# Performance work log

Measured on AMD Instinct MI355X. Metric: run time of the kernel, lower is better.

## Reference

```python
import jax, jax.numpy as jnp
import numpy as np


def setup_inputs() -> dict:
    key = jax.random.key(0)
    k1, k2 = jax.random.split(key)
    B, S, D, R = 8, 2048, 1024, 128
    batch = jax.random.normal(k1, (B, S, D), dtype=jnp.float32)
    proj = jax.random.normal(k2, (D, R), dtype=jnp.float32) * (1.0 / np.sqrt(D))
    return {"batch": batch, "proj": proj}


def reference(batch, proj):
    # transformed: (B, S, R)
    t = jnp.matmul(batch, proj)
    # Pairwise squared L2 distances: ||ti||^2 + ||tj||^2 - 2 ti.tj
    # (same math as expand/diff/pow/sum, without the (B,S,S,R) intermediate)
    sq = jnp.sum(t * t, axis=-1)                       # (B, S)
    dots = jnp.einsum('bir,bjr->bij', t, t)            # (B, S, S)
    d2 = sq[:, :, None] + sq[:, None, :] - 2.0 * dots  # (B, S, S)
    return d2
```

## Files before the change

kernel.cpp:

```cpp
#include <hip/hip_runtime.h>
#include <hip/hip_bf16.h>

typedef short bf16x8 __attribute__((ext_vector_type(8)));
typedef float f32x4 __attribute__((ext_vector_type(4)));

#define NB 8
#define SS 2048
#define DD 1024
#define RR 128

__device__ __forceinline__ short f2bf(float x){
  unsigned u = __float_as_uint(x);
  u += 0x7fffu + ((u >> 16) & 1u);
  return (short)(u >> 16);
}
__device__ __forceinline__ float bf2f(short h){
  return __uint_as_float(((unsigned)(unsigned short)h) << 16);
}
__device__ __forceinline__ void gload16(const void* g, void* l){
  __builtin_amdgcn_global_load_lds((const __attribute__((address_space(1))) unsigned*)g,
                                   (__attribute__((address_space(3))) unsigned*)l, 16, 0, 0);
}
__device__ __forceinline__ int swz(int row, int c16){
  return row * 64 + ((c16 ^ (row & 7)) << 3);
}

__global__ __launch_bounds__(256) void k0_proj(const float* __restrict__ proj,
                                               short* __restrict__ pt_hi,
                                               short* __restrict__ pt_lo){
  __shared__ float tile[64][65];
  const int d0 = blockIdx.x * 64, r0 = blockIdx.y * 64;
  const int tid = threadIdx.x;
  #pragma unroll
  for (int i = 0; i < 16; ++i){
    int u = i * 256 + tid;
    int d = u >> 6, r = u & 63;
    tile[d][r] = proj[(d0 + d) * RR + r0 + r];
  }
  __syncthreads();
  #pragma unroll
  for (int i = 0; i < 16; ++i){
    int u = i * 256 + tid;
    int r = u >> 6, d = u & 63;
    float x = tile[d][r];
    short h = f2bf(x);
    short l = f2bf(x - bf2f(h));
    pt_hi[(r0 + r) * DD + d0 + d] = h;
    pt_lo[(r0 + r) * DD + d0 + d] = l;
  }
}

__global__ __launch_bounds__(512, 2) void k1_gemm1(const float* __restrict__ batch,
                                                   const short* __restrict__ pt_hi,
                                                   const short* __restrict__ pt_lo,
                                                   short* __restrict__ t_hi,
                                                   float* __restrict__ sqv){
  __shared__ __align__(16) char smem[49408];
  short* Ah = (short*)smem;
  short* Al = (short*)(smem + 8192);
  short* Ph = (short*)(smem + 16384);
  short* Pl = (short*)(smem + 32768);
  float* sqpart = (float*)(smem + 49152);
  const int tid = threadIdx.x;
  const int w = tid >> 6, lane = tid & 63;
  const int lr = lane & 15, lg = lane >> 4;
  const int wr = w & 3, wc = w >> 2;
  const int row0 = blockIdx.x * 64;
  const int colg = (lane & 7) ^ (lane >> 3);
  if (tid < 64) sqpart[tid] = 0.f;
  f32x4 acc[4] = {{0.f,0.f,0.f,0.f}};
  #pragma unroll 1
  for (int k0 = 0; k0 < DD; k0 += 64){
    #pragma unroll
    for (int i = 0; i < 2; ++i){
      int u = tid * 2 + i;
      int r = u >> 4, kc = (u & 15) * 4;
      float4 v = *(const float4*)(batch + (size_t)(row0 + r) * DD + k0 + kc);
      short4 hv, lv;
      hv.x = f2bf(v.x); lv.x = f2bf(v.x - bf2f(hv.x));
      hv.y = f2bf(v.y); lv.y = f2bf(v.y - bf2f(hv.y));
      hv.z = f2bf(v.z); lv.z = f2bf(v.z - bf2f(hv.z));
      hv.w = f2bf(v.w); lv.w = f2bf(v.w - bf2f(hv.w));
      int sidx = r * 64 + (((kc >> 3) ^ (r & 7)) << 3) + (kc & 7);
      *(short4*)&Ah[sidx] = hv;
      *(short4*)&Al[sidx] = lv;
    }
    #pragma unroll
    for (int q = 0; q < 2; ++q){
      int prow = w * 16 + q * 8 + (lane >> 3);
      gload16(pt_hi + prow * DD + k0 + colg * 8, &Ph[w * 1024 + q * 512]);
      gload16(pt_lo + prow * DD + k0 + colg * 8, &Pl[w * 1024 + q * 512]);
    }
    __syncthreads();
    #pragma unroll
    for (int ks = 0; ks < 2; ++ks){
      int c16 = ks * 4 + lg;
      bf16x8 ah = *(const bf16x8*)&Ah[swz(wr * 16 + lr, c16)];
      bf16x8 al = *(const bf16x8*)&Al[swz(wr * 16 + lr, c16)];
      bf16x8 bh[4], bl[4];
      #pragma unroll
      for (int n = 0; n < 4; ++n){
        int prow = wc * 64 + n * 16 + lr;
        bh[n] = *(const bf16x8*)&Ph[swz(prow, c16)];
        bl[n] = *(const bf16x8*)&Pl[swz(prow, c16)];
      }
      #pragma unroll
      for (int n = 0; n < 4; ++n)
        acc[n] = __builtin_amdgcn_mfma_f32_16x16x32_bf16(ah, bh[n], acc[n], 0, 0, 0);
      #pragma unroll
      for (int n = 0; n < 4; ++n)
        acc[n] = __builtin_amdgcn_mfma_f32_16x16x32_bf16(ah, bl[n], acc[n], 0, 0, 0);
      #pragma unroll
      for (int n = 0; n < 4; ++n)
        acc[n] = __builtin_amdgcn_mfma_f32_16x16x32_bf16(al, bh[n], acc[n], 0, 0, 0);
    }
    __syncthreads();
  }
  short* Th = Ph;
  #pragma unroll
  for (int r = 0; r < 4; ++r){
    int lrow = wr * 16 + lg * 4 + r;
    float s = 0.f;
    #pragma unroll
    for (int n = 0; n < 4; ++n){
      float x = acc[n][r];
      s += x * x;
      int col = wc * 64 + n * 16 + lr;
      Th[lrow * 128 + col] = f2bf(x);
    }
    s += __shfl_xor(s, 1);
    s += __shfl_xor(s, 2);
    s += __shfl_xor(s, 4);
    s += __shfl_xor(s, 8);
    if (lr == 0) atomicAdd(&sqpart[lrow], s);
  }
  __syncthreads();
  #pragma unroll
  for (int ps = 0; ps < 2; ++ps){
    int u = ps * 512 + tid;
    int row = u >> 4, c8 = (u & 15) * 8;
    *(int4*)&t_hi[(size_t)(row0 + row) * RR + c8] = *(int4*)&Th[row * 128 + c8];
  }
  if (tid < 64) sqv[row0 + tid] = sqpart[tid];
}

__global__ __launch_bounds__(512, 4) void k2_dist(const short* __restrict__ t_hi,
                                                  const float* __restrict__ sqv,
                                                  float* __restrict__ out){
  __shared__ __align__(16) short lds[32768];
  float* ftile = (float*)lds;
  const int tid = threadIdx.x;
  const int w = tid >> 6, lane = tid & 63;
  const int lr = lane & 15, lg = lane >> 4;
  const int bi = blockIdx.x;
  int p = blockIdx.y;
  int ti = 0;
  while (p >= 16 - ti){ p -= 16 - ti; ++ti; }
  const int tj = ti + p;
  const int i0 = ti * 128, j0 = tj * 128;
  const bool dg = (ti == tj);
  const size_t tbase = (size_t)bi * SS * RR;
  float* outb = out + (size_t)bi * SS * SS;
  const float* sqb = sqv + bi * SS;
  const int srow = ((w & 1) << 2) | (lane >> 4);
  const int colg = (lane & 15) ^ srow;

  #pragma unroll
  for (int q = 0; q < 4; ++q){
    int rl = q * 32 + w * 4;
    int gr = rl + (lane >> 4);
    gload16(t_hi + tbase + (size_t)(i0 + gr) * RR + colg * 8, &lds[rl * 128]);
    if (!dg)
      gload16(t_hi + tbase + (size_t)(j0 + gr) * RR + colg * 8, &lds[16384 + rl * 128]);
  }
  __syncthreads();

  const int bh0 = dg ? 0 : 16384;
  f32x4 acc[8] = {{0.f,0.f,0.f,0.f}};
  const int ar = w * 16 + lr;
  const int aoff = ar * 128;
  const int asw = ar & 7;
  #pragma unroll
  for (int ks = 0; ks < 4; ++ks){
    int c16 = ks * 4 + lg;
    bf16x8 ah = *(const bf16x8*)&lds[aoff + ((c16 ^ asw) << 3)];
    bf16x8 bh[8];
    #pragma unroll
    for (int n = 0; n < 8; ++n){
      int br = n * 16 + lr;
      bh[n] = *(const bf16x8*)&lds[bh0 + br * 128 + ((c16 ^ (br & 7)) << 3)];
    }
    #pragma unroll
    for (int n = 0; n < 8; ++n)
      acc[n] = __builtin_amdgcn_mfma_f32_16x16x32_bf16(ah, bh[n], acc[n], 0, 0, 0);
  }
  __syncthreads();

  if (!dg){
    int rbase = w * 16 + lg * 4;
    float4 si4 = *(const float4*)&sqb[i0 + rbase];
    #pragma unroll
    for (int n = 0; n < 8; ++n){
      int col = n * 16 + lr;
      float sj = sqb[j0 + col];
      float4 mv;
      mv.x = si4.x + sj - 2.0f * acc[n][0];
      mv.y = si4.y + sj - 2.0f * acc[n][1];
      mv.z = si4.z + sj - 2.0f * acc[n][2];
      mv.w = si4.w + sj - 2.0f * acc[n][3];
      *(float4*)&outb[(size_t)(j0 + col) * SS + (i0 + rbase)] = mv;
    }
  }
  #pragma unroll
  for (int n = 0; n < 8; ++n)
    #pragma unroll
    for (int r = 0; r < 4; ++r)
      ftile[(w * 16 + lg * 4 + r) * 128 + n * 16 + lr] = acc[n][r];
  __syncthreads();
  #pragma unroll
  for (int v = 0; v < 8; ++v){
    int u = v * 512 + tid;
    int row = u >> 5, c4 = (u & 31) * 4;
    float4 d = *(float4*)&ftile[row * 128 + c4];
    float si = sqb[i0 + row];
    float4 sj = *(const float4*)&sqb[j0 + c4];
    float4 o;
    o.x = si + sj.x - 2.0f * d.x;
    o.y = si + sj.y - 2.0f * d.y;
    o.z = si + sj.z - 2.0f * d.z;
    o.w = si + sj.w - 2.0f * d.w;
    *(float4*)&outb[(size_t)(i0 + row) * SS + j0 + c4] = o;
  }
}

extern "C" void kernel_launch(void* const* d_in, const int* in_sizes, int n_in,
                              void* d_out, int out_size, void* d_ws, size_t ws_size,
                              hipStream_t stream) {
  const float* batch = (const float*)d_in[0];
  const float* proj  = (const float*)d_in[1];
  float* out = (float*)d_out;
  char* ws = (char*)d_ws;

  short* pt_hi = (short*)(ws);
  short* pt_lo = (short*)(ws + 262144);
  short* t_hi  = (short*)(ws + 524288);
  float* sqv   = (float*)(ws + 4718592);

  k0_proj<<<dim3(16, 2), 256, 0, stream>>>(proj, pt_hi, pt_lo);
  k1_gemm1<<<dim3(256), 512, 0, stream>>>(batch, pt_hi, pt_lo, t_hi, sqv);
  k2_dist<<<dim3(8, 136), 512, 0, stream>>>(t_hi, sqv, out);
}
```

Baseline: 207.9 us.

## Fuse three kernels into one cooperative persistent kernel with double-buffered GEMM

After: 360.7 us. 1.74x slower.

```diff
diff --git a/kernel.cpp b/kernel.cpp
--- a/kernel.cpp
+++ b/kernel.cpp
@@ -1,10 +1,12 @@
 #include <hip/hip_runtime.h>
 #include <hip/hip_bf16.h>
+#include <hip/hip_cooperative_groups.h>
+
+namespace cg = cooperative_groups;
 
 typedef short bf16x8 __attribute__((ext_vector_type(8)));
 typedef float f32x4 __attribute__((ext_vector_type(4)));
 
-#define NB 8
 #define SS 2048
 #define DD 1024
 #define RR 128
@@ -25,211 +27,238 @@
   return row * 64 + ((c16 ^ (row & 7)) << 3);
 }
 
-__global__ __launch_bounds__(256) void k0_proj(const float* __restrict__ proj,
-                                               short* __restrict__ pt_hi,
-                                               short* __restrict__ pt_lo){
-  __shared__ float tile[64][65];
-  const int d0 = blockIdx.x * 64, r0 = blockIdx.y * 64;
-  const int tid = threadIdx.x;
-  #pragma unroll
-  for (int i = 0; i < 16; ++i){
-    int u = i * 256 + tid;
-    int d = u >> 6, r = u & 63;
-    tile[d][r] = proj[(d0 + d) * RR + r0 + r];
-  }
-  __syncthreads();
-  #pragma unroll
-  for (int i = 0; i < 16; ++i){
-    int u = i * 256 + tid;
-    int r = u >> 6, d = u & 63;
-    float x = tile[d][r];
-    short h = f2bf(x);
-    short l = f2bf(x - bf2f(h));
-    pt_hi[(r0 + r) * DD + d0 + d] = h;
-    pt_lo[(r0 + r) * DD + d0 + d] = l;
-  }
-}
-
-__global__ __launch_bounds__(512, 2) void k1_gemm1(const float* __restrict__ batch,
-                                                   const short* __restrict__ pt_hi,
-                                                   const short* __restrict__ pt_lo,
-                                                   short* __restrict__ t_hi,
-                                                   float* __restrict__ sqv){
-  __shared__ __align__(16) char smem[49408];
-  short* Ah = (short*)smem;
-  short* Al = (short*)(smem + 8192);
-  short* Ph = (short*)(smem + 16384);
-  short* Pl = (short*)(smem + 32768);
-  float* sqpart = (float*)(smem + 49152);
+__global__ __launch_bounds__(512, 1) void fused_psd(
+    const float* __restrict__ batch, const float* __restrict__ proj,
+    short* __restrict__ pt_hi, short* __restrict__ pt_lo,
+    short* __restrict__ t_hi, float* __restrict__ sqv,
+    float* __restrict__ out){
+  __shared__ __align__(16) char smem[98560];
+  cg::grid_group grid = cg::this_grid();
+  const int b = blockIdx.x;
   const int tid = threadIdx.x;
   const int w = tid >> 6, lane = tid & 63;
   const int lr = lane & 15, lg = lane >> 4;
-  const int wr = w & 3, wc = w >> 2;
-  const int row0 = blockIdx.x * 64;
-  const int colg = (lane & 7) ^ (lane >> 3);
-  if (tid < 64) sqpart[tid] = 0.f;
-  f32x4 acc[4] = {{0.f,0.f,0.f,0.f}};
-  #pragma unroll 1
-  for (int k0 = 0; k0 < DD; k0 += 64){
-    #pragma unroll
-    for (int i = 0; i < 2; ++i){
-      int u = tid * 2 + i;
-      int r = u >> 4, kc = (u & 15) * 4;
-      float4 v = *(const float4*)(batch + (size_t)(row0 + r) * DD + k0 + kc);
-      short4 hv, lv;
-      hv.x = f2bf(v.x); lv.x = f2bf(v.x - bf2f(hv.x));
-      hv.y = f2bf(v.y); lv.y = f2bf(v.y - bf2f(hv.y));
-      hv.z = f2bf(v.z); lv.z = f2bf(v.z - bf2f(hv.z));
-      hv.w = f2bf(v.w); lv.w = f2bf(v.w - bf2f(hv.w));
-      int sidx = r * 64 + (((kc >> 3) ^ (r & 7)) << 3) + (kc & 7);
-      *(short4*)&Ah[sidx] = hv;
-      *(short4*)&Al[sidx] = lv;
-    }
-    #pragma unroll
-    for (int q = 0; q < 2; ++q){
-      int prow = w * 16 + q * 8 + (lane >> 3);
-      gload16(pt_hi + prow * DD + k0 + colg * 8, &Ph[w * 1024 + q * 512]);
-      gload16(pt_lo + prow * DD + k0 + colg * 8, &Pl[w * 1024 + q * 512]);
+
+  if (b < 32){
+    float* ftile = (float*)smem;
+    const int d0 = (b & 15) * 64, r0 = (b >> 4) * 64;
+    #pragma unroll
+    for (int i = 0; i < 8; ++i){
+      int u = i * 512 + tid;
+      int d = u >> 6, r = u & 63;
+      ftile[d * 65 + r] = proj[(d0 + d) * RR + r0 + r];
     }
     __syncthreads();
     #pragma unroll
-    for (int ks = 0; ks < 2; ++ks){
-      int c16 = ks * 4 + lg;
-      bf16x8 ah = *(const bf16x8*)&Ah[swz(wr * 16 + lr, c16)];
-      bf16x8 al = *(const bf16x8*)&Al[swz(wr * 16 + lr, c16)];
-      bf16x8 bh[4], bl[4];
+    for (int i = 0; i < 8; ++i){
+      int u = i * 512 + tid;
+      int r = u >> 6, d = u & 63;
+      float x = ftile[d * 65 + r];
+      short h = f2bf(x);
+      short l = f2bf(x - bf2f(h));
+      pt_hi[(r0 + r) * DD + d0 + d] = h;
+      pt_lo[(r0 + r) * DD + d0 + d] = l;
+    }
+  }
+  __threadfence();
+  grid.sync();
+
+  {
+    const int wr = w & 3, wc = w >> 2;
+    const int row0 = b * 64;
+    const int colg = (lane & 7) ^ (lane >> 3);
+    float* sqpart = (float*)(smem + 98304);
+    if (tid < 64) sqpart[tid] = 0.f;
+    f32x4 acc[4] = {{0.f,0.f,0.f,0.f}};
+    const int arow = tid >> 3;
+    const int akc = (tid & 7) * 8;
+    const int asidx = arow * 64 + (((akc >> 3) ^ (arow & 7)) << 3);
+
+    {
+      float4 v0 = *(const float4*)(batch + (size_t)(row0 + arow) * DD + akc);
+      float4 v1 = *(const float4*)(batch + (size_t)(row0 + arow) * DD + akc + 4);
+      short hv[8], lv[8];
+      float xs[8] = {v0.x,v0.y,v0.z,v0.w,v1.x,v1.y,v1.z,v1.w};
+      #pragma unroll
+      for (int e = 0; e < 8; ++e){ hv[e] = f2bf(xs[e]); lv[e] = f2bf(xs[e] - bf2f(hv[e])); }
+      *(short4*)((short*)smem + asidx)            = make_short4(hv[0],hv[1],hv[2],hv[3]);
+      *(short4*)((short*)smem + asidx + 4)        = make_short4(hv[4],hv[5],hv[6],hv[7]);
+      *(short4*)((short*)(smem+8192) + asidx)     = make_short4(lv[0],lv[1],lv[2],lv[3]);
+      *(short4*)((short*)(smem+8192) + asidx + 4) = make_short4(lv[4],lv[5],lv[6],lv[7]);
+      #pragma unroll
+      for (int q = 0; q < 2; ++q){
+        int prow = w * 16 + q * 8 + (lane >> 3);
+        gload16(pt_hi + prow * DD + colg * 8, (short*)(smem + 32768) + w * 1024 + q * 512);
+        gload16(pt_lo + prow * DD + colg * 8, (short*)(smem + 49152) + w * 1024 + q * 512);
+      }
+      __syncthreads();
+    }
+    #pragma unroll 1
+    for (int t = 0; t < 16; ++t){
+      const int cur = t & 1;
+      char* curA = smem + cur * 16384;
+      char* curP = smem + 32768 + cur * 32768;
+      char* nxtA = smem + (cur ^ 1) * 16384;
+      char* nxtP = smem + 32768 + (cur ^ 1) * 32768;
+      const bool pre = (t < 15);
+      float4 pv0, pv1;
+      if (pre){
+        const int kn = (t + 1) * 64;
+        pv0 = *(const float4*)(batch + (size_t)(row0 + arow) * DD + kn + akc);
+        pv1 = *(const float4*)(batch + (size_t)(row0 + arow) * DD + kn + akc + 4);
+        #pragma unroll
+        for (int q = 0; q < 2; ++q){
+          int prow = w * 16 + q * 8 + (lane >> 3);
+          gload16(pt_hi + prow * DD + kn + colg * 8, (short*)nxtP + w * 1024 + q * 512);
+          gload16(pt_lo + prow * DD + kn + colg * 8, (short*)(nxtP + 16384) + w * 1024 + q * 512);
+        }
+      }
+      #pragma unroll
+      for (int ks = 0; ks < 2; ++ks){
+        int c16 = ks * 4 + lg;
+        bf16x8 ah = *(const bf16x8*)((short*)curA + swz(wr * 16 + lr, c16));
+        bf16x8 al = *(const bf16x8*)((short*)(curA + 8192) + swz(wr * 16 + lr, c16));
+        bf16x8 bh[4], bl[4];
+        #pragma unroll
+        for (int n = 0; n < 4; ++n){
+          int prow = wc * 64 + n * 16 + lr;
+          bh[n] = *(const bf16x8*)((short*)curP + swz(prow, c16));
+          bl[n] = *(const bf16x8*)((short*)(curP + 16384) + swz(prow, c16));
+        }
+        #pragma unroll
+        for (int n = 0; n < 4; ++n)
+          acc[n] = __builtin_amdgcn_mfma_f32_16x16x32_bf16(ah, bh[n], acc[n], 0, 0, 0);
+        #pragma unroll
+        for (int n = 0; n < 4; ++n)
+          acc[n] = __builtin_amdgcn_mfma_f32_16x16x32_bf16(ah, bl[n], acc[n], 0, 0, 0);
+        #pragma unroll
+        for (int n = 0; n < 4; ++n)
+          acc[n] = __builtin_amdgcn_mfma_f32_16x16x32_bf16(al, bh[n], acc[n], 0, 0, 0);
+      }
+      if (pre){
+        short hv[8], lv[8];
+        float xs[8] = {pv0.x,pv0.y,pv0.z,pv0.w,pv1.x,pv1.y,pv1.z,pv1.w};
+        #pragma unroll
+        for (int e = 0; e < 8; ++e){ hv[e] = f2bf(xs[e]); lv[e] = f2bf(xs[e] - bf2f(hv[e])); }
+        *(short4*)((short*)nxtA + asidx)            = make_short4(hv[0],hv[1],hv[2],hv[3]);
+        *(short4*)((short*)nxtA + asidx + 4)        = make_short4(hv[4],hv[5],hv[6],hv[7]);
+        *(short4*)((short*)(nxtA+8192) + asidx)     = make_short4(lv[0],lv[1],lv[2],lv[3]);
+        *(short4*)((short*)(nxtA+8192) + asidx + 4) = make_short4(lv[4],lv[5],lv[6],lv[7]);
+      }
+      __syncthreads();
+    }
+    short* Th = (short*)(smem + 32768);
+    #pragma unroll
+    for (int r = 0; r < 4; ++r){
+      int lrow = wr * 16 + lg * 4 + r;
+      float s = 0.f;
       #pragma unroll
       for (int n = 0; n < 4; ++n){
-        int prow = wc * 64 + n * 16 + lr;
-        bh[n] = *(const bf16x8*)&Ph[swz(prow, c16)];
-        bl[n] = *(const bf16x8*)&Pl[swz(prow, c16)];
-      }
-      #pragma unroll
-      for (int n = 0; n < 4; ++n)
-        acc[n] = __builtin_amdgcn_mfma_f32_16x16x32_bf16(ah, bh[n], acc[n], 0, 0, 0);
-      #pragma unroll
-      for (int n = 0; n < 4; ++n)
-        acc[n] = __builtin_amdgcn_mfma_f32_16x16x32_bf16(ah, bl[n], acc[n], 0, 0, 0);
-      #pragma unroll
-      for (int n = 0; n < 4; ++n)
-        acc[n] = __builtin_amdgcn_mfma_f32_16x16x32_bf16(al, bh[n], acc[n], 0, 0, 0);
+        float x = acc[n][r];
+        s += x * x;
+        Th[lrow * 128 + wc * 64 + n * 16 + lr] = f2bf(x);
+      }
+      s += __shfl_xor(s, 1);
+      s += __shfl_xor(s, 2);
+      s += __shfl_xor(s, 4);
+      s += __shfl_xor(s, 8);
+      if (lr == 0) atomicAdd(&sqpart[lrow], s);
     }
     __syncthreads();
+    #pragma unroll
+    for (int ps = 0; ps < 2; ++ps){
+      int u = ps * 512 + tid;
+      int row = u >> 4, c8 = (u & 15) * 8;
+      *(int4*)&t_hi[(size_t)(row0 + row) * RR + c8] = *(int4*)&Th[row * 128 + c8];
+    }
+    if (tid < 64) sqv[row0 + tid] = sqpart[tid];
   }
-  short* Th = Ph;
-  #pragma unroll
-  for (int r = 0; r < 4; ++r){
-    int lrow = wr * 16 + lg * 4 + r;
-    float s = 0.f;
-    #pragma unroll
-    for (int n = 0; n < 4; ++n){
-      float x = acc[n][r];
-      s += x * x;
-      int col = wc * 64 + n * 16 + lr;
-      Th[lrow * 128 + col] = f2bf(x);
-    }
-    s += __shfl_xor(s, 1);
-    s += __shfl_xor(s, 2);
-    s += __shfl_xor(s, 4);
-    s += __shfl_xor(s, 8);
-    if (lr == 0) atomicAdd(&sqpart[lrow], s);
-  }
-  __syncthreads();
-  #pragma unroll
-  for (int ps = 0; ps < 2; ++ps){
-    int u = ps * 512 + tid;
-    int row = u >> 4, c8 = (u & 15) * 8;
-    *(int4*)&t_hi[(size_t)(row0 + row) * RR + c8] = *(int4*)&Th[row * 128 + c8];
-  }
-  if (tid < 64) sqv[row0 + tid] = sqpart[tid];
-}
-
-__global__ __launch_bounds__(512, 4) void k2_dist(const short* __restrict__ t_hi,
-                                                  const float* __restrict__ sqv,
-                                                  float* __restrict__ out){
-  __shared__ __align__(16) short lds[32768];
-  float* ftile = (float*)lds;
-  const int tid = threadIdx.x;
-  const int w = tid >> 6, lane = tid & 63;
-  const int lr = lane & 15, lg = lane >> 4;
-  const int bi = blockIdx.x;
-  int p = blockIdx.y;
-  int ti = 0;
-  while (p >= 16 - ti){ p -= 16 - ti; ++ti; }
-  const int tj = ti + p;
-  const int i0 = ti * 128, j0 = tj * 128;
-  const bool dg = (ti == tj);
-  const size_t tbase = (size_t)bi * SS * RR;
-  float* outb = out + (size_t)bi * SS * SS;
-  const float* sqb = sqv + bi * SS;
-  const int srow = ((w & 1) << 2) | (lane >> 4);
-  const int colg = (lane & 15) ^ srow;
-
-  #pragma unroll
-  for (int q = 0; q < 4; ++q){
-    int rl = q * 32 + w * 4;
-    int gr = rl + (lane >> 4);
-    gload16(t_hi + tbase + (size_t)(i0 + gr) * RR + colg * 8, &lds[rl * 128]);
-    if (!dg)
-      gload16(t_hi + tbase + (size_t)(j0 + gr) * RR + colg * 8, &lds[16384 + rl * 128]);
-  }
-  __syncthreads();
-
-  const int bh0 = dg ? 0 : 16384;
-  f32x4 acc[8] = {{0.f,0.f,0.f,0.f}};
-  const int ar = w * 16 + lr;
-  const int aoff = ar * 128;
-  const int asw = ar & 7;
-  #pragma unroll
-  for (int ks = 0; ks < 4; ++ks){
-    int c16 = ks * 4 + lg;
-    bf16x8 ah = *(const bf16x8*)&lds[aoff + ((c16 ^ asw) << 3)];
-    bf16x8 bh[8];
-    #pragma unroll
-    for (int n = 0; n < 8; ++n){
-      int br = n * 16 + lr;
-      bh[n] = *(const bf16x8*)&lds[bh0 + br * 128 + ((c16 ^ (br & 7)) << 3)];
-    }
-    #pragma unroll
-    for (int n = 0; n < 8; ++n)
-      acc[n] = __builtin_amdgcn_mfma_f32_16x16x32_bf16(ah, bh[n], acc[n], 0, 0, 0);
-  }
-  __syncthreads();
-
-  if (!dg){
-    int rbase = w * 16 + lg * 4;
-    float4 si4 = *(const float4*)&sqb[i0 + rbase];
-    #pragma unroll
-    for (int n = 0; n < 8; ++n){
-      int col = n * 16 + lr;
-      float sj = sqb[j0 + col];
-      float4 mv;
-      mv.x = si4.x + sj - 2.0f * acc[n][0];
-      mv.y = si4.y + sj - 2.0f * acc[n][1];
-      mv.z = si4.z + sj - 2.0f * acc[n][2];
-      mv.w = si4.w + sj - 2.0f * acc[n][3];
-      *(float4*)&outb[(size_t)(j0 + col) * SS + (i0 + rbase)] = mv;
-    }
-  }
-  #pragma unroll
-  for (int n = 0; n < 8; ++n)
-    #pragma unroll
-    for (int r = 0; r < 4; ++r)
-      ftile[(w * 16 + lg * 4 + r) * 128 + n * 16 + lr] = acc[n][r];
-  __syncthreads();
-  #pragma unroll
-  for (int v = 0; v < 8; ++v){
-    int u = v * 512 + tid;
-    int row = u >> 5, c4 = (u & 31) * 4;
-    float4 d = *(float4*)&ftile[row * 128 + c4];
-    float si = sqb[i0 + row];
-    float4 sj = *(const float4*)&sqb[j0 + c4];
-    float4 o;
-    o.x = si + sj.x - 2.0f * d.x;
-    o.y = si + sj.y - 2.0f * d.y;
-    o.z = si + sj.z - 2.0f * d.z;
-    o.w = si + sj.w - 2.0f * d.w;
-    *(float4*)&outb[(size_t)(i0 + row) * SS + j0 + c4] = o;
+  __threadfence();
+  grid.sync();
+
+  {
+    const int bi = b & 7;
+    const int lidx = b >> 3;
+    const size_t tbase = (size_t)bi * SS * RR;
+    float* outb = out + (size_t)bi * SS * SS;
+    const float* sqb = sqv + bi * SS;
+    const int srow = ((w & 1) << 2) | (lane >> 4);
+    const int colg2 = (lane & 15) ^ srow;
+    short* ldsA = (short*)smem;
+    short* ldsB = (short*)(smem + 32768);
+    float* ftile = (float*)smem;
+    #pragma unroll 1
+    for (int pp = lidx; pp < 136; pp += 32){
+      int p = pp, ti = 0;
+      while (p >= 16 - ti){ p -= 16 - ti; ++ti; }
+      const int tj = ti + p;
+      const int i0 = ti * 128, j0 = tj * 128;
+      const bool dg = (ti == tj);
+      __syncthreads();
+      #pragma unroll
+      for (int q = 0; q < 4; ++q){
+        int rl = q * 32 + w * 4;
+        int gr = rl + (lane >> 4);
+        gload16(t_hi + tbase + (size_t)(i0 + gr) * RR + colg2 * 8, &ldsA[rl * 128]);
+        if (!dg)
+          gload16(t_hi + tbase + (size_t)(j0 + gr) * RR + colg2 * 8, &ldsB[rl * 128]);
+      }
+      __syncthreads();
+      short* ldsBB = dg ? ldsA : ldsB;
+      f32x4 acc[8] = {{0.f,0.f,0.f,0.f}};
+      const int ar = w * 16 + lr;
+      const int aoff = ar * 128, asw = ar & 7;
+      #pragma unroll
+      for (int ks = 0; ks < 4; ++ks){
+        int c16 = ks * 4 + lg;
+        bf16x8 ah = *(const bf16x8*)&ldsA[aoff + ((c16 ^ asw) << 3)];
+        bf16x8 bh[8];
+        #pragma unroll
+        for (int n = 0; n < 8; ++n){
+          int br = n * 16 + lr;
+          bh[n] = *(const bf16x8*)&ldsBB[br * 128 + ((c16 ^ (br & 7)) << 3)];
+        }
+        #pragma unroll
+        for (int n = 0; n < 8; ++n)
+          acc[n] = __builtin_amdgcn_mfma_f32_16x16x32_bf16(ah, bh[n], acc[n], 0, 0, 0);
+      }
+      __syncthreads();
+      if (!dg){
+        int rbase = w * 16 + lg * 4;
+        float4 si4 = *(const float4*)&sqb[i0 + rbase];
+        #pragma unroll
+        for (int n = 0; n < 8; ++n){
+          int col = n * 16 + lr;
+          float sj = sqb[j0 + col];
+          float4 mv;
+          mv.x = si4.x + sj - 2.0f * acc[n][0];
+          mv.y = si4.y + sj - 2.0f * acc[n][1];
+          mv.z = si4.z + sj - 2.0f * acc[n][2];
+          mv.w = si4.w + sj - 2.0f * acc[n][3];
+          *(float4*)&outb[(size_t)(j0 + col) * SS + (i0 + rbase)] = mv;
+        }
+      }
+      #pragma unroll
+      for (int n = 0; n < 8; ++n)
+        #pragma unroll
+        for (int r = 0; r < 4; ++r)
+          ftile[(w * 16 + lg * 4 + r) * 128 + n * 16 + lr] = acc[n][r];
+      __syncthreads();
+      #pragma unroll
+      for (int v = 0; v < 8; ++v){
+        int u = v * 512 + tid;
+        int row = u >> 5, c4 = (u & 31) * 4;
+        float4 d = *(float4*)&ftile[row * 128 + c4];
+        float si = sqb[i0 + row];
+        float4 sj = *(const float4*)&sqb[j0 + c4];
+        float4 o;
+        o.x = si + sj.x - 2.0f * d.x;
+        o.y = si + sj.y - 2.0f * d.y;
+        o.z = si + sj.z - 2.0f * d.z;
+        o.w = si + sj.w - 2.0f * d.w;
+        *(float4*)&outb[(size_t)(i0 + row) * SS + j0 + c4] = o;
+      }
+    }
   }
 }
 
@@ -246,7 +275,13 @@
   short* t_hi  = (short*)(ws + 524288);
   float* sqv   = (float*)(ws + 4718592);
 
-  k0_proj<<<dim3(16, 2), 256, 0, stream>>>(proj, pt_hi, pt_lo);
-  k1_gemm1<<<dim3(256), 512, 0, stream>>>(batch, pt_hi, pt_lo, t_hi, sqv);
-  k2_dist<<<dim3(8, 136), 512, 0, stream>>>(t_hi, sqv, out);
-}
+  void* args[7];
+  args[0] = (void*)&batch;
+  args[1] = (void*)&proj;
+  args[2] = (void*)&pt_hi;
+  args[3] = (void*)&pt_lo;
+  args[4] = (void*)&t_hi;
+  args[5] = (void*)&sqv;
+  args[6] = (void*)&out;
+  hipLaunchCooperativeKernel(fused_psd, dim3(256), dim3(512), args, 0, stream);
+}
```
